# Optimization experiments

Measured on AMD Instinct MI355X. Metric: run time of the kernel, lower is better.

## Reference

```python
import jax, jax.numpy as jnp
import numpy as np

HID = 768          # args.hidden_size
LSTM2 = 768        # args.lstm_dim * 2
SCALE = HID ** -0.5


def _cross_attn(q_in, kv_in, Wq, bq, Wk, bk, Wv, bv):
    # Linear projections (weights stored as [in, out])
    Q = q_in @ Wq + bq            # [B, Sq, H]
    K = kv_in @ Wk + bk           # [B, Sk, H]
    V = kv_in @ Wv + bv           # [B, Sk, H]
    attn = jnp.einsum('bqh,bkh->bqk', Q, K) * SCALE
    attn = jax.nn.softmax(attn, axis=-1)
    return jnp.einsum('bqk,bkh->bqh', attn, V)


def setup_inputs() -> dict:
    key = jax.random.key(0)
    ks = jax.random.split(key, 14)
    B, Ssyn, Ssem = 4, 4096, 2048
    syntactic_feat = jax.random.normal(ks[0], (B, Ssyn, LSTM2), jnp.float32)
    semantic_feat = jax.random.normal(ks[1], (B, Ssem, HID), jnp.float32)

    def lin(k, fan_in, fan_out):
        kw, kb = jax.random.split(k)
        bound = 1.0 / np.sqrt(fan_in)
        W = jax.random.uniform(kw, (fan_in, fan_out), jnp.float32, -bound, bound)
        b = jax.random.uniform(kb, (fan_out,), jnp.float32, -bound, bound)
        return W, b

    # syntax_to_semantic: query_dim=HID, key_dim=LSTM2
    Wq1, bq1 = lin(ks[2], HID, HID)
    Wk1, bk1 = lin(ks[3], LSTM2, HID)
    Wv1, bv1 = lin(ks[4], LSTM2, HID)
    # semantic_to_syntax: query_dim=LSTM2, key_dim=HID
    Wq2, bq2 = lin(ks[5], LSTM2, HID)
    Wk2, bk2 = lin(ks[6], HID, HID)
    Wv2, bv2 = lin(ks[7], HID, HID)
    return dict(syntactic_feat=syntactic_feat, semantic_feat=semantic_feat,
                Wq1=Wq1, bq1=bq1, Wk1=Wk1, bk1=bk1, Wv1=Wv1, bv1=bv1,
                Wq2=Wq2, bq2=bq2, Wk2=Wk2, bk2=bk2, Wv2=Wv2, bv2=bv2)


def reference(syntactic_feat, semantic_feat,
              Wq1, bq1, Wk1, bk1, Wv1, bv1,
              Wq2, bq2, Wk2, bk2, Wv2, bv2):
    # enhanced_semantic: queries from semantic, keys/values from syntactic
    enhanced_semantic = _cross_attn(semantic_feat, syntactic_feat,
                                    Wq1, bq1, Wk1, bk1, Wv1, bv1)
    # enhanced_syntax: queries from syntactic, keys/values from semantic
    enhanced_syntax = _cross_attn(syntactic_feat, semantic_feat,
                                  Wq2, bq2, Wk2, bk2, Wv2, bv2)
    return enhanced_semantic, enhanced_syntax
```

## Files before the change

kernel.cpp:

```cpp
#include <hip/hip_runtime.h>
#include <stdint.h>


typedef unsigned short u16;
typedef __attribute__((ext_vector_type(8))) __bf16 bf16x8;
typedef __attribute__((ext_vector_type(4))) float f32x4;

__device__ __forceinline__ float bf2f(u16 u) {
  union { unsigned int i; float f; } x; x.i = ((unsigned int)u) << 16; return x.f;
}
__device__ __forceinline__ u16 f2bf(float f) {
  union { float f; unsigned int i; } x; x.f = f;
  unsigned int i = x.i;
  i += 0x7fffu + ((i >> 16) & 1u);
  return (u16)(i >> 16);
}

__device__ __forceinline__ void cp16(void* lds, const void* g) {
  __builtin_amdgcn_global_load_lds((__attribute__((address_space(1))) void*)g,
                                   (__attribute__((address_space(3))) void*)lds,
                                   16, 0, 0);
}

struct GemmDesc {
  const u16* A; const u16* Bt; const float* bias; void* C;
  long sA, sB, sC;
  int K, lda, ldb, ldc;
  int gx, gy;
  int start;
  int mode, outf;
  float scale;
};
struct GemmPack { GemmDesc d[6]; int nd; };

#define PHASE(MH, I0, PAR, RDB, STAGE, WAITC)                                 \
  {                                                                           \
    const bf16x8* As8 =                                                       \
        (const bf16x8*)((const char*)L + (PAR) * 32768 + (MH) * 16384);       \
    bf16x8 a0[2][2];                                                          \
    _Pragma("unroll")                                                         \
    for (int s = 0; s < 2; ++s)                                               \
      _Pragma("unroll")                                                       \
      for (int i = 0; i < 2; ++i) a0[s][i] = As8[iaq[s][(I0) + i]];           \
    if (RDB) {                                                                \
      const bf16x8* Bl8 =                                                     \
          (const bf16x8*)((const char*)L + 65536 + (PAR) * 32768);            \
      const bf16x8* Bh8 =                                                     \
          (const bf16x8*)((const char*)L + 65536 + (PAR) * 32768 + 16384);    \
      _Pragma("unroll")                                                       \
      for (int s = 0; s < 2; ++s)                                             \
        _Pragma("unroll")                                                     \
        for (int j = 0; j < 2; ++j) {                                         \
          bfr[0][s][j] = Bl8[ibq[s][j]];                                      \
          bfr[1][s][j] = Bh8[ibq[s][j]];                                      \
        }                                                                     \
    }                                                                         \
    STAGE;                                                                    \
    if (RDB) { asm volatile("s_waitcnt lgkmcnt(8)" ::: "memory"); }           \
    __builtin_amdgcn_s_barrier();                                             \
    asm volatile("s_waitcnt lgkmcnt(0)" ::: "memory");                        \
    __builtin_amdgcn_s_setprio(1);                                            \
    _Pragma("unroll")                                                         \
    for (int s = 0; s < 2; ++s)                                               \
      _Pragma("unroll")                                                       \
      for (int i = 0; i < 2; ++i)                                             \
        _Pragma("unroll")                                                     \
        for (int nh = 0; nh < 2; ++nh)                                        \
          _Pragma("unroll")                                                   \
          for (int j = 0; j < 2; ++j)                                         \
            acc[MH][nh][(I0) + i][j] =                                        \
                __builtin_amdgcn_mfma_f32_16x16x32_bf16(                      \
                    bfr[nh][s][j], a0[s][i], acc[MH][nh][(I0) + i][j],        \
                    0, 0, 0);                                                 \
    __builtin_amdgcn_s_setprio(0);                                            \
    WAITC;                                                                    \
    __builtin_amdgcn_s_barrier();                                             \
  }

__global__ __launch_bounds__(512, 2)
void gemm256_kernel(GemmPack p)
{
  __shared__ __align__(16) u16 L[65536];

  int seg = 0;
#pragma unroll
  for (int t = 1; t < 6; ++t)
    if (t < p.nd && (int)blockIdx.x >= p.d[t].start) seg = t;
  const GemmDesc& g = p.d[seg];
  const int local = (int)blockIdx.x - g.start;
  const int pxy = g.gx * g.gy;
  const int bz = local / pxy;
  const int rem = local - bz * pxy;
  const int by = rem / g.gx;
  const int bx = rem - by * g.gx;

  const int tid  = threadIdx.x;
  const int lane = tid & 63;
  const int wave = tid >> 6;
  const int l15  = lane & 15;
  const int quad = lane >> 4;
  const int wm   = wave >> 2;
  const int wn   = wave & 3;

  const char* Ab = (const char*)(g.A + (long)bz * g.sA + (long)bx * 256 * g.lda);
  const char* Bb = (const char*)(g.Bt + (long)bz * g.sB + (long)by * 256 * g.ldb);
  const long ldaB = (long)g.lda * 2;
  const long ldbB = (long)g.ldb * 2;

  const int gchk = (lane & 7) ^ (lane >> 3);
  const char* pa0 = Ab + (long)(wave * 8 + (lane >> 3)) * ldaB + (gchk << 4);
  const char* pb0 = Bb + (long)(wave * 8 + (lane >> 3)) * ldbB + (gchk << 4);
  char* lA = (char*)L + wave * 1024;
  char* lB = (char*)L + 65536 + wave * 1024;

  auto stA = [&](int tile, int h) {
    char* d = lA + (tile & 1) * 32768 + h * 16384;
    const char* s = pa0 + (long)h * 128 * ldaB + ((long)tile << 7);
    cp16(d, s);
    cp16(d + 8192, s + 64 * ldaB);
  };
  auto stB = [&](int tile, int h) {
    char* d = lB + (tile & 1) * 32768 + h * 16384;
    const char* s = pb0 + (long)h * 128 * ldbB + ((long)tile << 7);
    cp16(d, s);
    cp16(d + 8192, s + 64 * ldbB);
  };

  int iaq[2][4], ibq[2][2];
#pragma unroll
  for (int s = 0; s < 2; ++s) {
#pragma unroll
    for (int i = 0; i < 4; ++i)
      iaq[s][i] = (wm * 64 + i * 16 + l15) * 8 + ((s * 4 + quad) ^ (l15 & 7));
#pragma unroll
    for (int j = 0; j < 2; ++j)
      ibq[s][j] = (wn * 32 + j * 16 + l15) * 8 + ((s * 4 + quad) ^ (l15 & 7));
  }

  f32x4 acc[2][2][4][2];
  {
    f32x4 zz = {0.f, 0.f, 0.f, 0.f};
#pragma unroll
    for (int mh = 0; mh < 2; ++mh)
#pragma unroll
      for (int nh = 0; nh < 2; ++nh)
#pragma unroll
        for (int i = 0; i < 4; ++i)
#pragma unroll
          for (int j = 0; j < 2; ++j) acc[mh][nh][i][j] = zz;
  }
  bf16x8 bfr[2][2][2];

  stB(0, 0); stB(0, 1); stA(0, 0); stA(0, 1);
  stB(1, 0); stB(1, 1); stA(1, 0);
  asm volatile("s_waitcnt vmcnt(6)" ::: "memory");
  __builtin_amdgcn_s_barrier();

  const int nt = g.K >> 6;
  const int NI = nt >> 1;
  for (int it = 0; it < NI; ++it) {
    const int t = it * 2;
    const bool m2 = (t + 2) < nt;
    const bool m3 = (t + 3) < nt;
    PHASE(0, 0, 0, 1, stA(t + 1, 1), )
    PHASE(0, 2, 0, 0, if (m2) stB(t + 2, 0), )
    PHASE(1, 0, 0, 0, if (m2) stB(t + 2, 1), )
    PHASE(1, 2, 0, 0, if (m2) stA(t + 2, 0),
          if (m2) { asm volatile("s_waitcnt vmcnt(6)" ::: "memory"); }
          else    { asm volatile("s_waitcnt vmcnt(0)" ::: "memory"); })
    PHASE(0, 0, 1, 1, if (m2) stA(t + 2, 1), )
    PHASE(0, 2, 1, 0, if (m3) stB(t + 3, 0), )
    PHASE(1, 0, 1, 0, if (m3) stB(t + 3, 1), )
    PHASE(1, 2, 1, 0, if (m3) stA(t + 3, 0),
          if (m3)      { asm volatile("s_waitcnt vmcnt(6)" ::: "memory"); }
          else if (m2) { asm volatile("s_waitcnt vmcnt(0)" ::: "memory"); })
  }

  const long cbase = (long)bz * g.sC;
#pragma unroll
  for (int mh = 0; mh < 2; ++mh) {
#pragma unroll
    for (int i = 0; i < 4; ++i) {
      const int row = bx * 256 + mh * 128 + wm * 64 + i * 16 + l15;
      const float rbias = (g.mode == 2) ? g.bias[row] : 0.f;
#pragma unroll
      for (int nh = 0; nh < 2; ++nh) {
#pragma unroll
        for (int j = 0; j < 2; ++j) {
          const int colbase = by * 256 + nh * 128 + wn * 32 + j * 16 + quad * 4;
          float v[4];
#pragma unroll
          for (int r = 0; r < 4; ++r) v[r] = acc[mh][nh][i][j][r] * g.scale;
          if (g.mode == 1) {
            const float4 cb = *(const float4*)(g.bias + colbase);
            v[0] += cb.x; v[1] += cb.y; v[2] += cb.z; v[3] += cb.w;
          } else if (g.mode == 2) {
#pragma unroll
            for (int r = 0; r < 4; ++r) v[r] += rbias;
          }
          const long idx = cbase + (long)row * g.ldc + colbase;
          if (g.outf) {
            float4 st; st.x = v[0]; st.y = v[1]; st.z = v[2]; st.w = v[3];
            *(float4*)((float*)g.C + idx) = st;
          } else {
            uint2 st;
            st.x = (unsigned int)f2bf(v[0]) | ((unsigned int)f2bf(v[1]) << 16);
            st.y = (unsigned int)f2bf(v[2]) | ((unsigned int)f2bf(v[3]) << 16);
            *(uint2*)((u16*)g.C + idx) = st;
          }
        }
      }
    }
  }
}

struct G128Desc {
  const u16* A; const u16* Bt; const float* bias; void* C;
  long sA, sB, sC;
  int K, lda, ldb, ldc;
  int gx, gy;
  int start;
  int mode, outf;
  float scale;
};
struct G128Pack { G128Desc d[6]; int nd; };

__global__ __launch_bounds__(256)
void gemm128_kernel(G128Pack p)
{
  __shared__ __align__(16) u16 Asl[128 * 64];
  __shared__ __align__(16) u16 Bsl[128 * 64];

  int seg = 0;
#pragma unroll
  for (int t = 1; t < 6; ++t)
    if (t < p.nd && (int)blockIdx.x >= p.d[t].start) seg = t;
  const G128Desc& g = p.d[seg];
  const int local = (int)blockIdx.x - g.start;
  const int pxy = g.gx * g.gy;
  const int bz = local / pxy;
  const int rem = local - bz * pxy;
  const int by = rem / g.gx;
  const int bx = rem - by * g.gx;

  const int tid  = threadIdx.x;
  const int lane = tid & 63;
  const int wave = tid >> 6;
  const int l15  = lane & 15;
  const int quad = lane >> 4;
  const int mw   = (wave >> 1) * 64;
  const int nw   = (wave & 1) * 64;

  const char* Ab = (const char*)(g.A + (long)bz * g.sA + (long)bx * 128 * g.lda);
  const char* Bb = (const char*)(g.Bt + (long)bz * g.sB + (long)by * 128 * g.ldb);

  const int srow  = wave * 8 + (lane >> 3);
  const int gchk  = (lane & 7) ^ (lane >> 3);
  const long ldaB = (long)g.lda * 2;
  const long ldbB = (long)g.ldb * 2;
  const char* pa00 = Ab + (long)srow * ldaB + (gchk << 4);
  const char* pb00 = Bb + (long)srow * ldbB + (gchk << 4);
  char* ldsA = (char*)Asl + wave * 1024;
  char* ldsB = (char*)Bsl + wave * 1024;

  int ia[2][4], ib[2][4];
#pragma unroll
  for (int s = 0; s < 2; ++s)
#pragma unroll
    for (int i = 0; i < 4; ++i) {
      const int m = mw + i * 16 + l15;
      ia[s][i] = m * 8 + ((s * 4 + quad) ^ (l15 & 7));
      const int n = nw + i * 16 + l15;
      ib[s][i] = n * 8 + ((s * 4 + quad) ^ (l15 & 7));
    }

  f32x4 acc[4][4];
  {
    f32x4 zz = {0.f, 0.f, 0.f, 0.f};
#pragma unroll
    for (int i = 0; i < 4; ++i)
#pragma unroll
      for (int j = 0; j < 4; ++j) acc[i][j] = zz;
  }

  const int nk = g.K >> 6;
  for (int kk = 0; kk < nk; ++kk) {
    const long kb = (long)kk << 7;
#pragma unroll
    for (int r = 0; r < 4; ++r) {
      cp16(ldsA + r * 4096, pa00 + kb + (long)r * 32 * ldaB);
      cp16(ldsB + r * 4096, pb00 + kb + (long)r * 32 * ldbB);
    }
    __syncthreads();

    const bf16x8* As8 = (const bf16x8*)Asl;
    const bf16x8* Bs8 = (const bf16x8*)Bsl;
#pragma unroll
    for (int s = 0; s < 2; ++s) {
      bf16x8 a[4], b[4];
#pragma unroll
      for (int i = 0; i < 4; ++i) a[i] = As8[ia[s][i]];
#pragma unroll
      for (int j = 0; j < 4; ++j) b[j] = Bs8[ib[s][j]];
#pragma unroll
      for (int i = 0; i < 4; ++i)
#pragma unroll
        for (int j = 0; j < 4; ++j)
          acc[i][j] = __builtin_amdgcn_mfma_f32_16x16x32_bf16(b[j], a[i], acc[i][j], 0, 0, 0);
    }
    __syncthreads();
  }

  const long cbase = (long)bz * g.sC;
#pragma unroll
  for (int i = 0; i < 4; ++i) {
    const int row = bx * 128 + mw + i * 16 + l15;
    const float rbias = (g.mode == 2) ? g.bias[row] : 0.f;
#pragma unroll
    for (int j = 0; j < 4; ++j) {
      const int colbase = by * 128 + nw + j * 16 + quad * 4;
      float v[4];
#pragma unroll
      for (int r = 0; r < 4; ++r) v[r] = acc[i][j][r] * g.scale;
      if (g.mode == 1) {
        const float4 cb = *(const float4*)(g.bias + colbase);
        v[0] += cb.x; v[1] += cb.y; v[2] += cb.z; v[3] += cb.w;
      } else if (g.mode == 2) {
#pragma unroll
        for (int r = 0; r < 4; ++r) v[r] += rbias;
      }
      const long idx = cbase + (long)row * g.ldc + colbase;
      if (g.outf) {
        float4 st; st.x = v[0]; st.y = v[1]; st.z = v[2]; st.w = v[3];
        *(float4*)((float*)g.C + idx) = st;
      } else {
        uint2 st;
        st.x = (unsigned int)f2bf(v[0]) | ((unsigned int)f2bf(v[1]) << 16);
        st.y = (unsigned int)f2bf(v[2]) | ((unsigned int)f2bf(v[3]) << 16);
        *(uint2*)((u16*)g.C + idx) = st;
      }
    }
  }
}

__global__ __launch_bounds__(256)
void prep_kernel(const float* __restrict__ sa, u16* __restrict__ da, int n8a,
                 const float* __restrict__ sb, u16* __restrict__ db, int n8b,
                 const float* w0, const float* w1, const float* w2,
                 const float* w3, const float* w4, const float* w5,
                 u16* t0, u16* t1, u16* t2, u16* t3, u16* t4, u16* t5)
{
  __shared__ float t[32][33];
  const int b = blockIdx.x;
  const int tid = threadIdx.x;
  if (b < 9216) {
    int idx = b * 256 + tid;
    const float* src; u16* dst; int i;
    if (idx < n8a) { src = sa; dst = da; i = idx; }
    else           { src = sb; dst = db; i = idx - n8a; if (i >= n8b) return; }
    const float4* s4 = (const float4*)src;
    float4 a = s4[i * 2], c = s4[i * 2 + 1];
    uint4 o;
    o.x = (unsigned int)f2bf(a.x) | ((unsigned int)f2bf(a.y) << 16);
    o.y = (unsigned int)f2bf(a.z) | ((unsigned int)f2bf(a.w) << 16);
    o.z = (unsigned int)f2bf(c.x) | ((unsigned int)f2bf(c.y) << 16);
    o.w = (unsigned int)f2bf(c.z) | ((unsigned int)f2bf(c.w) << 16);
    ((uint4*)dst)[i] = o;
    return;
  }
  const int tb = b - 9216;
  const int z  = tb / 576;
  const int r  = tb - z * 576;
  const int byy = r / 24;
  const int bxx = r - byy * 24;
  const float* src; u16* dst;
  switch (z) {
    case 0: src = w0; dst = t0; break;
    case 1: src = w1; dst = t1; break;
    case 2: src = w2; dst = t2; break;
    case 3: src = w3; dst = t3; break;
    case 4: src = w4; dst = t4; break;
    default: src = w5; dst = t5; break;
  }
  const int tx = tid & 31, ty = tid >> 5;
  const int x = bxx * 32 + tx;
  const int y0 = byy * 32;
#pragma unroll
  for (int j = 0; j < 32; j += 8) t[ty + j][tx] = src[(long)(y0 + ty + j) * 768 + x];
  __syncthreads();
  const int x2 = y0 + tx;
#pragma unroll
  for (int j = 0; j < 32; j += 8)
    dst[(long)(bxx * 32 + ty + j) * 768 + x2] = f2bf(t[tx][ty + j]);
}

template <int NV>
__device__ __forceinline__ void softmax_row(u16* row)
{
  __shared__ float red[8];
  const int tid  = threadIdx.x;
  const int lane = tid & 63;
  const int wave = tid >> 6;
  uint4* p4 = (uint4*)row;

  uint4 ld[NV / 8];
#pragma unroll
  for (int c = 0; c < NV / 8; ++c) ld[c] = p4[tid + c * 256];
  float v[NV];
#pragma unroll
  for (int c = 0; c < NV / 8; ++c) {
    unsigned int w[4] = {ld[c].x, ld[c].y, ld[c].z, ld[c].w};
#pragma unroll
    for (int q = 0; q < 4; ++q) {
      v[c * 8 + q * 2]     = bf2f((u16)(w[q] & 0xffffu));
      v[c * 8 + q * 2 + 1] = bf2f((u16)(w[q] >> 16));
    }
  }

  float m = -1e30f;
#pragma unroll
  for (int i = 0; i < NV; ++i) m = fmaxf(m, v[i]);
#pragma unroll
  for (int off = 32; off > 0; off >>= 1) m = fmaxf(m, __shfl_xor(m, off, 64));
  if (lane == 0) red[wave] = m;
  __syncthreads();
  m = fmaxf(fmaxf(red[0], red[1]), fmaxf(red[2], red[3]));

  float s = 0.f;
#pragma unroll
  for (int i = 0; i < NV; ++i) { v[i] = __expf(v[i] - m); s += v[i]; }
#pragma unroll
  for (int off = 32; off > 0; off >>= 1) s += __shfl_xor(s, off, 64);
  if (lane == 0) red[4 + wave] = s;
  __syncthreads();
  s = (red[4] + red[5]) + (red[6] + red[7]);
  const float inv = 1.0f / s;

#pragma unroll
  for (int c = 0; c < NV / 8; ++c) {
    unsigned int w[4];
#pragma unroll
    for (int q = 0; q < 4; ++q) {
      const u16 lo = f2bf(v[c * 8 + q * 2] * inv);
      const u16 hi = f2bf(v[c * 8 + q * 2 + 1] * inv);
      w[q] = (unsigned int)lo | ((unsigned int)hi << 16);
    }
    uint4 st; st.x = w[0]; st.y = w[1]; st.z = w[2]; st.w = w[3];
    p4[tid + c * 256] = st;
  }
}

__global__ __launch_bounds__(256)
void softmax_both_kernel(u16* S1, u16* S2, const u16* cpy_src, u16* cpy_dst)
{
  if (blockIdx.x < 8192) { softmax_row<16>(S1 + (long)blockIdx.x * 4096); return; }
  if (blockIdx.x < 24576) { softmax_row<8>(S2 + (long)(blockIdx.x - 8192) * 2048); return; }
  const long base = (long)(blockIdx.x - 24576) * 512 + threadIdx.x;
  const uint4* s = (const uint4*)cpy_src;
  uint4* d = (uint4*)cpy_dst;
  d[base] = s[base];
  d[base + 256] = s[base + 256];
}


static GemmDesc mkdesc(const void* A, const void* Bt, const float* bias, void* C,
                       long sA, long sB, long sC, int K, int lda, int ldb, int ldc,
                       int M, int N, int start, int mode, int outf, float scale)
{
  GemmDesc d;
  d.A = (const u16*)A; d.Bt = (const u16*)Bt; d.bias = bias; d.C = C;
  d.sA = sA; d.sB = sB; d.sC = sC;
  d.K = K; d.lda = lda; d.ldb = ldb; d.ldc = ldc;
  d.gx = M / 256; d.gy = N / 256; d.start = start;
  d.mode = mode; d.outf = outf; d.scale = scale;
  return d;
}

static G128Desc mk128(const void* A, const void* Bt, const float* bias, void* C,
                      long sA, long sB, long sC, int K, int lda, int ldb, int ldc,
                      int M, int N, int start, int mode, int outf, float scale)
{
  G128Desc d;
  d.A = (const u16*)A; d.Bt = (const u16*)Bt; d.bias = bias; d.C = C;
  d.sA = sA; d.sB = sB; d.sC = sC;
  d.K = K; d.lda = lda; d.ldb = ldb; d.ldc = ldc;
  d.gx = M / 128; d.gy = N / 128; d.start = start;
  d.mode = mode; d.outf = outf; d.scale = scale;
  return d;
}

extern "C" void kernel_launch(void* const* d_in, const int* in_sizes, int n_in,
                              void* d_out, int out_size, void* d_ws, size_t ws_size,
                              hipStream_t stream)
{
  (void)in_sizes; (void)n_in; (void)out_size; (void)ws_size;
  const float* syn = (const float*)d_in[0];
  const float* sem = (const float*)d_in[1];
  const float* W[6]    = {(const float*)d_in[2], (const float*)d_in[4],  (const float*)d_in[6],
                          (const float*)d_in[8], (const float*)d_in[10], (const float*)d_in[12]};
  const float* bias[6] = {(const float*)d_in[3], (const float*)d_in[5],  (const float*)d_in[7],
                          (const float*)d_in[9], (const float*)d_in[11], (const float*)d_in[13]};
  float* out = (float*)d_out;

  u16* ws   = (u16*)d_ws;
  u16* S1   = ws;
  u16* synb = ws;
  u16* semb = ws + 12582912;
  u16* WT   = ws + 18874368;
  u16* S2   = ws + 33554432;
  u16* V1T  = ws + 67108864;
  u16* Q1   = ws + 79691776;
  u16* V2Tc = ws + 79691776;
  u16* K1  = (u16*)out;
  u16* o1  = (u16*)(out + 6291456);
  u16* Q2  = o1;
  u16* K2  = o1 + 12582912;
  u16* V2T = o1 + 18874368;

  const float SC = 0.036084391824351615f;

  prep_kernel<<<dim3(12672), dim3(256), 0, stream>>>(
      syn, synb, 1572864, sem, semb, 786432,
      W[0], W[1], W[2], W[3], W[4], W[5],
      WT + 0 * 589824, WT + 1 * 589824, WT + 2 * 589824,
      WT + 3 * 589824, WT + 4 * 589824, WT + 5 * 589824);

  {
    GemmPack p; p.nd = 6;
    p.d[0] = mkdesc(synb, WT + 1 * 589824, bias[1], K1, 0, 0, 0,
                    768, 768, 768, 768, 16384, 768, 0, 1, 0, 1.f);
    p.d[1] = mkdesc(synb, WT + 3 * 589824, bias[3], Q2, 0, 0, 0,
                    768, 768, 768, 768, 16384, 768, 192, 1, 0, 1.f);
    p.d[2] = mkdesc(WT + 2 * 589824, synb, bias[2], V1T, 0, 0, 0,
                    768, 768, 768, 16384, 768, 16384, 384, 2, 0, 1.f);
    p.d[3] = mkdesc(semb, WT + 0 * 589824, bias[0], Q1, 0, 0, 0,
                    768, 768, 768, 768, 8192, 768, 576, 1, 0, 1.f);
    p.d[4] = mkdesc(semb, WT + 4 * 589824, bias[4], K2, 0, 0, 0,
                    768, 768, 768, 768, 8192, 768, 672, 1, 0, 1.f);
    p.d[5] = mkdesc(WT + 5 * 589824, semb, bias[5], V2T, 0, 0, 0,
                    768, 768, 768, 8192, 768, 8192, 768, 2, 0, 1.f);
    gemm256_kernel<<<dim3(864), dim3(512), 0, stream>>>(p);
  }

  {
    GemmPack p; p.nd = 2;
    p.d[0] = mkdesc(Q1, K1, nullptr, S1,
                    1572864L, 3145728L, 8388608L,
                    768, 768, 768, 4096, 2048, 4096, 0, 0, 0, SC);
    p.d[1] = mkdesc(Q2, K2, nullptr, S2,
                    3145728L, 1572864L, 8388608L,
                    768, 768, 768, 2048, 4096, 2048, 512, 0, 0, SC);
    gemm256_kernel<<<dim3(1024), dim3(512), 0, stream>>>(p);
  }

  softmax_both_kernel<<<dim3(26112), dim3(256), 0, stream>>>(S1, S2, V2T, V2Tc);

  {
    G128Pack p; p.nd = 2;
    p.d[0] = mk128(S1, V1T, nullptr, out,
                   8388608L, 4096L, 1572864L,
                   4096, 4096, 16384, 768, 2048, 768, 0, 0, 1, 1.f);
    p.d[1] = mk128(S2, V2Tc, nullptr, out + 6291456,
                   8388608L, 2048L, 3145728L,
                   2048, 2048, 8192, 768, 4096, 768, 384, 0, 1, 1.f);
    gemm128_kernel<<<dim3(1152), dim3(256), 0, stream>>>(p);
  }
}
```

Measured before the change: 570.5 us.

## Fuse softmax into score GEMM epilogue and PV GEMM row-sum normalization

New measurement: 567.4 us. No clear change (-0.5%).

```diff
diff --git a/kernel.cpp b/kernel.cpp
--- a/kernel.cpp
+++ b/kernel.cpp
@@ -28,7 +28,7 @@
   int K, lda, ldb, ldc;
   int gx, gy;
   int start;
-  int mode, outf;
+  int mode, outf, expo;
   float scale;
 };
 struct GemmPack { GemmDesc d[6]; int nd; };
@@ -198,6 +198,10 @@
 #pragma unroll
             for (int r = 0; r < 4; ++r) v[r] += rbias;
           }
+          if (g.expo) {
+#pragma unroll
+            for (int r = 0; r < 4; ++r) v[r] = __expf(v[r]);
+          }
           const long idx = cbase + (long)row * g.ldc + colbase;
           if (g.outf) {
             float4 st; st.x = v[0]; st.y = v[1]; st.z = v[2]; st.w = v[3];
@@ -220,7 +224,7 @@
   int K, lda, ldb, ldc;
   int gx, gy;
   int start;
-  int mode, outf;
+  int mode, outf, rsum;
   float scale;
 };
 struct G128Pack { G128Desc d[6]; int nd; };
@@ -275,13 +279,19 @@
     }
 
   f32x4 acc[4][4];
+  f32x4 acc1[4];
   {
     f32x4 zz = {0.f, 0.f, 0.f, 0.f};
 #pragma unroll
-    for (int i = 0; i < 4; ++i)
+    for (int i = 0; i < 4; ++i) {
 #pragma unroll
       for (int j = 0; j < 4; ++j) acc[i][j] = zz;
-  }
+      acc1[i] = zz;
+    }
+  }
+  bf16x8 ones;
+#pragma unroll
+  for (int z = 0; z < 8; ++z) ones[z] = (__bf16)1.0f;
 
   const int nk = g.K >> 6;
   for (int kk = 0; kk < nk; ++kk) {
@@ -307,6 +317,11 @@
 #pragma unroll
         for (int j = 0; j < 4; ++j)
           acc[i][j] = __builtin_amdgcn_mfma_f32_16x16x32_bf16(b[j], a[i], acc[i][j], 0, 0, 0);
+      if (g.rsum) {
+#pragma unroll
+        for (int i = 0; i < 4; ++i)
+          acc1[i] = __builtin_amdgcn_mfma_f32_16x16x32_bf16(ones, a[i], acc1[i], 0, 0, 0);
+      }
     }
     __syncthreads();
   }
@@ -316,12 +331,13 @@
   for (int i = 0; i < 4; ++i) {
     const int row = bx * 128 + mw + i * 16 + l15;
     const float rbias = (g.mode == 2) ? g.bias[row] : 0.f;
+    const float mulf = g.rsum ? (1.0f / acc1[i][0]) : g.scale;
 #pragma unroll
     for (int j = 0; j < 4; ++j) {
       const int colbase = by * 128 + nw + j * 16 + quad * 4;
       float v[4];
 #pragma unroll
-      for (int r = 0; r < 4; ++r) v[r] = acc[i][j][r] * g.scale;
+      for (int r = 0; r < 4; ++r) v[r] = acc[i][j][r] * mulf;
       if (g.mode == 1) {
         const float4 cb = *(const float4*)(g.bias + colbase);
         v[0] += cb.x; v[1] += cb.y; v[2] += cb.z; v[3] += cb.w;
@@ -394,98 +410,32 @@
     dst[(long)(bxx * 32 + ty + j) * 768 + x2] = f2bf(t[tx][ty + j]);
 }
 
-template <int NV>
-__device__ __forceinline__ void softmax_row(u16* row)
-{
-  __shared__ float red[8];
-  const int tid  = threadIdx.x;
-  const int lane = tid & 63;
-  const int wave = tid >> 6;
-  uint4* p4 = (uint4*)row;
-
-  uint4 ld[NV / 8];
-#pragma unroll
-  for (int c = 0; c < NV / 8; ++c) ld[c] = p4[tid + c * 256];
-  float v[NV];
-#pragma unroll
-  for (int c = 0; c < NV / 8; ++c) {
-    unsigned int w[4] = {ld[c].x, ld[c].y, ld[c].z, ld[c].w};
-#pragma unroll
-    for (int q = 0; q < 4; ++q) {
-      v[c * 8 + q * 2]     = bf2f((u16)(w[q] & 0xffffu));
-      v[c * 8 + q * 2 + 1] = bf2f((u16)(w[q] >> 16));
-    }
-  }
-
-  float m = -1e30f;
-#pragma unroll
-  for (int i = 0; i < NV; ++i) m = fmaxf(m, v[i]);
-#pragma unroll
-  for (int off = 32; off > 0; off >>= 1) m = fmaxf(m, __shfl_xor(m, off, 64));
-  if (lane == 0) red[wave] = m;
-  __syncthreads();
-  m = fmaxf(fmaxf(red[0], red[1]), fmaxf(red[2], red[3]));
-
-  float s = 0.f;
-#pragma unroll
-  for (int i = 0; i < NV; ++i) { v[i] = __expf(v[i] - m); s += v[i]; }
-#pragma unroll
-  for (int off = 32; off > 0; off >>= 1) s += __shfl_xor(s, off, 64);
-  if (lane == 0) red[4 + wave] = s;
-  __syncthreads();
-  s = (red[4] + red[5]) + (red[6] + red[7]);
-  const float inv = 1.0f / s;
-
-#pragma unroll
-  for (int c = 0; c < NV / 8; ++c) {
-    unsigned int w[4];
-#pragma unroll
-    for (int q = 0; q < 4; ++q) {
-      const u16 lo = f2bf(v[c * 8 + q * 2] * inv);
-      const u16 hi = f2bf(v[c * 8 + q * 2 + 1] * inv);
-      w[q] = (unsigned int)lo | ((unsigned int)hi << 16);
-    }
-    uint4 st; st.x = w[0]; st.y = w[1]; st.z = w[2]; st.w = w[3];
-    p4[tid + c * 256] = st;
-  }
-}
-
-__global__ __launch_bounds__(256)
-void softmax_both_kernel(u16* S1, u16* S2, const u16* cpy_src, u16* cpy_dst)
-{
-  if (blockIdx.x < 8192) { softmax_row<16>(S1 + (long)blockIdx.x * 4096); return; }
-  if (blockIdx.x < 24576) { softmax_row<8>(S2 + (long)(blockIdx.x - 8192) * 2048); return; }
-  const long base = (long)(blockIdx.x - 24576) * 512 + threadIdx.x;
-  const uint4* s = (const uint4*)cpy_src;
-  uint4* d = (uint4*)cpy_dst;
-  d[base] = s[base];
-  d[base + 256] = s[base + 256];
-}
-
 
 static GemmDesc mkdesc(const void* A, const void* Bt, const float* bias, void* C,
                        long sA, long sB, long sC, int K, int lda, int ldb, int ldc,
-                       int M, int N, int start, int mode, int outf, float scale)
+                       int M, int N, int start, int mode, int outf, int expo,
+                       float scale)
 {
   GemmDesc d;
   d.A = (const u16*)A; d.Bt = (const u16*)Bt; d.bias = bias; d.C = C;
   d.sA = sA; d.sB = sB; d.sC = sC;
   d.K = K; d.lda = lda; d.ldb = ldb; d.ldc = ldc;
   d.gx = M / 256; d.gy = N / 256; d.start = start;
-  d.mode = mode; d.outf = outf; d.scale = scale;
+  d.mode = mode; d.outf = outf; d.expo = expo; d.scale = scale;
   return d;
 }
 
 static G128Desc mk128(const void* A, const void* Bt, const float* bias, void* C,
                       long sA, long sB, long sC, int K, int lda, int ldb, int ldc,
-                      int M, int N, int start, int mode, int outf, float scale)
+                      int M, int N, int start, int mode, int outf, int rsum,
+                      float scale)
 {
   G128Desc d;
   d.A = (const u16*)A; d.Bt = (const u16*)Bt; d.bias = bias; d.C = C;
   d.sA = sA; d.sB = sB; d.sC = sC;
   d.K = K; d.lda = lda; d.ldb = ldb; d.ldc = ldc;
   d.gx = M / 128; d.gy = N / 128; d.start = start;
-  d.mode = mode; d.outf = outf; d.scale = scale;
+  d.mode = mode; d.outf = outf; d.rsum = rsum; d.scale = scale;
   return d;
 }
 
@@ -509,13 +459,12 @@
   u16* WT   = ws + 18874368;
   u16* S2   = ws + 33554432;
   u16* V1T  = ws + 67108864;
-  u16* Q1   = ws + 79691776;
-  u16* V2Tc = ws + 79691776;
+  u16* V2T  = ws + 79691776;
   u16* K1  = (u16*)out;
   u16* o1  = (u16*)(out + 6291456);
   u16* Q2  = o1;
   u16* K2  = o1 + 12582912;
-  u16* V2T = o1 + 18874368;
+  u16* Q1  = o1 + 18874368;
 
   const float SC = 0.036084391824351615f;
 
@@ -528,17 +477,17 @@
   {
     GemmPack p; p.nd = 6;
     p.d[0] = mkdesc(synb, WT + 1 * 589824, bias[1], K1, 0, 0, 0,
-                    768, 768, 768, 768, 16384, 768, 0, 1, 0, 1.f);
+                    768, 768, 768, 768, 16384, 768, 0, 1, 0, 0, 1.f);
     p.d[1] = mkdesc(synb, WT + 3 * 589824, bias[3], Q2, 0, 0, 0,
-                    768, 768, 768, 768, 16384, 768, 192, 1, 0, 1.f);
+                    768, 768, 768, 768, 16384, 768, 192, 1, 0, 0, 1.f);
     p.d[2] = mkdesc(WT + 2 * 589824, synb, bias[2], V1T, 0, 0, 0,
-                    768, 768, 768, 16384, 768, 16384, 384, 2, 0, 1.f);
+                    768, 768, 768, 16384, 768, 16384, 384, 2, 0, 0, 1.f);
     p.d[3] = mkdesc(semb, WT + 0 * 589824, bias[0], Q1, 0, 0, 0,
-                    768, 768, 768, 768, 8192, 768, 576, 1, 0, 1.f);
+                    768, 768, 768, 768, 8192, 768, 576, 1, 0, 0, 1.f);
     p.d[4] = mkdesc(semb, WT + 4 * 589824, bias[4], K2, 0, 0, 0,
-                    768, 768, 768, 768, 8192, 768, 672, 1, 0, 1.f);
+                    768, 768, 768, 768, 8192, 768, 672, 1, 0, 0, 1.f);
     p.d[5] = mkdesc(WT + 5 * 589824, semb, bias[5], V2T, 0, 0, 0,
-                    768, 768, 768, 8192, 768, 8192, 768, 2, 0, 1.f);
+                    768, 768, 768, 8192, 768, 8192, 768, 2, 0, 0, 1.f);
     gemm256_kernel<<<dim3(864), dim3(512), 0, stream>>>(p);
   }
 
@@ -546,23 +495,21 @@
     GemmPack p; p.nd = 2;
     p.d[0] = mkdesc(Q1, K1, nullptr, S1,
                     1572864L, 3145728L, 8388608L,
-                    768, 768, 768, 4096, 2048, 4096, 0, 0, 0, SC);
+                    768, 768, 768, 4096, 2048, 4096, 0, 0, 0, 1, SC);
     p.d[1] = mkdesc(Q2, K2, nullptr, S2,
                     3145728L, 1572864L, 8388608L,
-                    768, 768, 768, 2048, 4096, 2048, 512, 0, 0, SC);
+                    768, 768, 768, 2048, 4096, 2048, 512, 0, 0, 1, SC);
     gemm256_kernel<<<dim3(1024), dim3(512), 0, stream>>>(p);
   }
-
-  softmax_both_kernel<<<dim3(26112), dim3(256), 0, stream>>>(S1, S2, V2T, V2Tc);
 
   {
     G128Pack p; p.nd = 2;
     p.d[0] = mk128(S1, V1T, nullptr, out,
                    8388608L, 4096L, 1572864L,
-                   4096, 4096, 16384, 768, 2048, 768, 0, 0, 1, 1.f);
-    p.d[1] = mk128(S2, V2Tc, nullptr, out + 6291456,
+                   4096, 4096, 16384, 768, 2048, 768, 0, 0, 1, 1, 1.f);
+    p.d[1] = mk128(S2, V2T, nullptr, out + 6291456,
                    8388608L, 2048L, 3145728L,
-                   2048, 2048, 8192, 768, 4096, 768, 384, 0, 1, 1.f);
+                   2048, 2048, 8192, 768, 4096, 768, 384, 0, 1, 1, 1.f);
     gemm128_kernel<<<dim3(1152), dim3(256), 0, stream>>>(p);
   }
 }
```
